# Kernel optimization log

Measured on AMD Instinct MI355X. Metric: run time of the kernel, lower is better.

## Reference

```python
import jax, jax.numpy as jnp
import numpy as np

B, S, IN, OUT, SPLIT = 4, 2048, 4096, 4096, 1024


def setup_inputs() -> dict:
    key = jax.random.key(0)
    ks = jax.random.split(key, 14)
    def n(k, shape, scale=1.0):
        return jax.random.normal(k, shape, dtype=jnp.float32) * scale
    return {
        "x": n(ks[0], (B, S, IN)),
        "V": n(ks[1], (SPLIT, IN)),
        "U": n(ks[2], (OUT, SPLIT)),
        "v2": n(ks[3], (1, IN), 0.05),
        "v1": n(ks[4], (1, SPLIT), 0.05),
        "u2": n(ks[5], (1, SPLIT), 0.05),
        "u1": n(ks[6], (1, OUT), 0.05),
        "V_R": n(ks[7], (SPLIT, IN)),
        "U_R": n(ks[8], (OUT, SPLIT)),
        "v2_R": n(ks[9], (1, IN), 0.05),
        "v1_R": n(ks[10], (1, SPLIT), 0.05),
        "u2_R": n(ks[11], (1, SPLIT), 0.05),
        "u1_R": n(ks[12], (1, OUT), 0.05),
        "bias": n(ks[13], (OUT,), 0.02),
    }


def _quantize(w):
    # ITQ binarization: sign(w) with straight-through estimator semantics
    return w + jax.lax.stop_gradient(jnp.sign(w) - w)


def _compute_forward(x2d, V, U, v2, v1, u2, u1):
    # x2d: [T, in]; V: [split, in]; U: [out, split]
    Vq = _quantize(V)
    Uq = _quantize(U)
    v1u2 = v1 * u2  # [1, split]
    h = (x2d * v2) @ Vq.T          # [T, split]
    return (h * v1u2) @ Uq.T * u1  # [T, out]


def reference(x, V, U, v2, v1, u2, u1, V_R, U_R, v2_R, v1_R, u2_R, u1_R, bias):
    lead = x.shape[:-1]
    x2d = x.reshape(-1, x.shape[-1])
    y = _compute_forward(x2d, V, U, v2, v1, u2, u1)
    y = y + _compute_forward(x2d, V_R, U_R, v2_R, v1_R, u2_R, u1_R)
    y = y + bias
    return y.reshape(lead + (U.shape[0],))
```

## Files before the change

### kernel.cpp

```cpp
#include <hip/hip_runtime.h>


typedef __bf16 bf16x8 __attribute__((ext_vector_type(8)));
typedef float floatx4 __attribute__((ext_vector_type(4)));

__device__ __forceinline__ unsigned short f2bf_rne(float f) {
    union { float f; unsigned u; } v; v.f = f;
    unsigned r = v.u + 0x7FFFu + ((v.u >> 16) & 1u);
    return (unsigned short)(r >> 16);
}

__device__ __forceinline__ float sgnf(float w) {
    return (float)((w > 0.f) - (w < 0.f));
}

__device__ __forceinline__ void async_copy16(const void* g, void* l) {
    __builtin_amdgcn_global_load_lds(
        (const __attribute__((address_space(1))) void*)g,
        (__attribute__((address_space(3))) void*)l, 16, 0, 0);
}

#define FENCE() asm volatile("" ::: "memory")
#define BAR() do { FENCE(); __builtin_amdgcn_s_barrier(); FENCE(); } while (0)
#define VMW(N) asm volatile("s_waitcnt vmcnt(" #N ")" ::: "memory")
#define LGKM(N) asm volatile("s_waitcnt lgkmcnt(" #N ")" ::: "memory")


__global__ void cast_x_kernel(const float* __restrict__ x,
                              unsigned short* __restrict__ xb, int n4) {
    int i = blockIdx.x * blockDim.x + threadIdx.x;
    if (i >= n4) return;
    float4 v = ((const float4*)x)[i];
    ushort4 o;
    o.x = f2bf_rne(v.x); o.y = f2bf_rne(v.y);
    o.z = f2bf_rne(v.z); o.w = f2bf_rne(v.w);
    ((ushort4*)xb)[i] = o;
}

__global__ void prep_w_kernel(const float* __restrict__ V, const float* __restrict__ V_R,
                              const float* __restrict__ v2, const float* __restrict__ v2_R,
                              const float* __restrict__ U, const float* __restrict__ U_R,
                              const float* __restrict__ v1, const float* __restrict__ v1_R,
                              const float* __restrict__ u2, const float* __restrict__ u2_R,
                              const float* __restrict__ u1, const float* __restrict__ u1_R,
                              unsigned short* __restrict__ W1,
                              unsigned short* __restrict__ W2) {
    int bid = blockIdx.x;
    if (bid < 8192) {
        int i = bid * blockDim.x + threadIdx.x;
        int idx = i << 2;
        int scat = idx >> 12;
        int k = idx & 4095;
        const float* Vp; const float* sp;
        if (scat < 1024) { Vp = V + ((size_t)scat << 12); sp = v2; }
        else             { Vp = V_R + ((size_t)(scat - 1024) << 12); sp = v2_R; }
        float4 w = *(const float4*)(Vp + k);
        float4 s = *(const float4*)(sp + k);
        ushort4 o;
        o.x = f2bf_rne(sgnf(w.x) * s.x);
        o.y = f2bf_rne(sgnf(w.y) * s.y);
        o.z = f2bf_rne(sgnf(w.z) * s.z);
        o.w = f2bf_rne(sgnf(w.w) * s.w);
        ((ushort4*)W1)[i] = o;
    } else {
        int i = (bid - 8192) * blockDim.x + threadIdx.x;
        int idx = i << 2;
        int o = idx >> 11;
        int scat = idx & 2047;
        int branch = scat >> 10;
        int s = scat & 1023;
        const float* Up  = branch ? U_R  : U;
        const float* v1p = branch ? v1_R : v1;
        const float* u2p = branch ? u2_R : u2;
        float u1v = (branch ? u1_R : u1)[o];
        float4 w = *(const float4*)(Up + ((size_t)o << 10) + s);
        float4 a = *(const float4*)(v1p + s);
        float4 b = *(const float4*)(u2p + s);
        ushort4 out;
        out.x = f2bf_rne(sgnf(w.x) * a.x * b.x * u1v);
        out.y = f2bf_rne(sgnf(w.y) * a.y * b.y * u1v);
        out.z = f2bf_rne(sgnf(w.z) * a.z * b.z * u1v);
        out.w = f2bf_rne(sgnf(w.w) * a.w * b.w * u1v);
        ((ushort4*)W2)[i] = out;
    }
}


template <bool OUT_BF16, bool ADD_BIAS>
__global__ __launch_bounds__(512, 2)
void gemm256(const unsigned short* __restrict__ A,
             const unsigned short* __restrict__ B,
             void* __restrict__ Cv,
             const float* __restrict__ bias,
             int M, int N, int K, int ntn) {
    (void)M;
    __shared__ __align__(16) unsigned short As[2][2][128 * 64];
    __shared__ __align__(16) unsigned short Bs[2][2][128 * 64];

    const int tid = threadIdx.x;
    const int lane = tid & 63;
    const int wave = tid >> 6;
    const int warp_m = wave >> 2;
    const int warp_n = wave & 3;

    const int nwg = gridDim.x;
    const int hw = blockIdx.x;
    const int swz = (hw & 7) * (nwg >> 3) + (hw >> 3);
    const int tm = swz / ntn;
    const int tn = swz - tm * ntn;
    const int m0 = tm << 8;
    const int n0 = tn << 8;

    const int srow = tid >> 3;
    const int scg8 = (((tid & 7) ^ (srow & 7)) << 3);
    const int ldst = tid << 3;
    const size_t Ks = (size_t)K;

    auto stA = [&](int buf, int h, int kt) {
        const unsigned short* g = A + (size_t)(m0 + (h << 7) + srow) * Ks + (kt << 6) + scg8;
        async_copy16(g,             &As[buf][h][ldst]);
        async_copy16(g + (Ks << 6), &As[buf][h][4096 + ldst]);
    };
    auto stB = [&](int buf, int h, int kt) {
        const unsigned short* g = B + (size_t)(n0 + (h << 7) + srow) * Ks + (kt << 6) + scg8;
        async_copy16(g,             &Bs[buf][h][ldst]);
        async_copy16(g + (Ks << 6), &Bs[buf][h][4096 + ldst]);
    };

    const int fm = lane & 15;
    const int cgl = lane >> 4;
    const int key = fm & 7;
    const int ok0 = ((cgl ^ key) << 3);
    const int ok1 = (((4 | cgl) ^ key) << 3);

    auto lda = [&](bf16x8 (&dst)[4][2], int buf, int mh) {
        const unsigned short* base = &As[buf][warp_m][0];
#pragma unroll
        for (int mi = 0; mi < 4; ++mi) {
            const unsigned short* p = base + (((mh << 6) + (mi << 4) + fm) << 6);
            dst[mi][0] = *(const bf16x8*)(p + ok0);
            dst[mi][1] = *(const bf16x8*)(p + ok1);
        }
    };
    auto ldb = [&](bf16x8 (&dst)[2][2], int buf, int nh) {
        const unsigned short* base = &Bs[buf][warp_n >> 1][0];
#pragma unroll
        for (int ni = 0; ni < 2; ++ni) {
            const unsigned short* p = base + ((((warp_n & 1) << 6) + (nh << 5) + (ni << 4) + fm) << 6);
            dst[ni][0] = *(const bf16x8*)(p + ok0);
            dst[ni][1] = *(const bf16x8*)(p + ok1);
        }
    };

    floatx4 acc[8][4];
#pragma unroll
    for (int i = 0; i < 8; ++i)
#pragma unroll
        for (int j = 0; j < 4; ++j)
#pragma unroll
            for (int r = 0; r < 4; ++r) acc[i][j][r] = 0.f;

    bf16x8 a0[4][2], a1[4][2], b0[2][2], b1[2][2];

#define MMAQ(aS, bS, MH, NH) do { \
    __builtin_amdgcn_s_setprio(1); \
    _Pragma("unroll") \
    for (int mi_ = 0; mi_ < 4; ++mi_) { \
      _Pragma("unroll") \
      for (int ni_ = 0; ni_ < 2; ++ni_) { \
        acc[(MH)*4 + mi_][(NH)*2 + ni_] = __builtin_amdgcn_mfma_f32_16x16x32_bf16( \
            aS[mi_][0], bS[ni_][0], acc[(MH)*4 + mi_][(NH)*2 + ni_], 0, 0, 0); \
        acc[(MH)*4 + mi_][(NH)*2 + ni_] = __builtin_amdgcn_mfma_f32_16x16x32_bf16( \
            aS[mi_][1], bS[ni_][1], acc[(MH)*4 + mi_][(NH)*2 + ni_], 0, 0, 0); \
      } } \
    __builtin_amdgcn_s_setprio(0); \
  } while (0)

    stB(0, 0, 0); stB(0, 1, 0); stA(0, 0, 0); stA(0, 1, 0);
    stB(1, 0, 1); stB(1, 1, 1); stA(1, 0, 1); stA(1, 1, 1);
    VMW(8);
    BAR();

    const int NT = K >> 6;
    for (int i = 0; i < (NT >> 1) - 1; ++i) {
        const int t2k = 2 * i + 2, t3k = 2 * i + 3;
        lda(a0, 0, 0); ldb(b0, 0, 0);
        BAR(); LGKM(0);
        MMAQ(a0, b0, 0, 0);
        BAR();
        ldb(b1, 0, 1);
        BAR(); LGKM(0);
        MMAQ(a0, b1, 0, 1);
        BAR();
        lda(a1, 0, 1);
        stB(0, 0, t2k); stB(0, 1, t2k);
        BAR(); LGKM(0);
        MMAQ(a1, b1, 1, 1);
        BAR();
        stA(0, 0, t2k); stA(0, 1, t2k);
        VMW(8);
        BAR();
        MMAQ(a1, b0, 1, 0);
        BAR();
        lda(a0, 1, 0); ldb(b0, 1, 0);
        BAR(); LGKM(0);
        MMAQ(a0, b0, 0, 0);
        BAR();
        ldb(b1, 1, 1);
        BAR(); LGKM(0);
        MMAQ(a0, b1, 0, 1);
        BAR();
        lda(a1, 1, 1);
        stB(1, 0, t3k); stB(1, 1, t3k);
        BAR(); LGKM(0);
        MMAQ(a1, b1, 1, 1);
        BAR();
        stA(1, 0, t3k); stA(1, 1, t3k);
        VMW(8);
        BAR();
        MMAQ(a1, b0, 1, 0);
        BAR();
    }
    {
        lda(a0, 0, 0); ldb(b0, 0, 0);
        BAR(); LGKM(0);
        MMAQ(a0, b0, 0, 0);
        BAR();
        ldb(b1, 0, 1);
        BAR(); LGKM(0);
        MMAQ(a0, b1, 0, 1);
        BAR();
        lda(a1, 0, 1);
        BAR(); LGKM(0);
        MMAQ(a1, b1, 1, 1);
        BAR();
        VMW(0);
        BAR();
        MMAQ(a1, b0, 1, 0);
        BAR();
        lda(a0, 1, 0); ldb(b0, 1, 0);
        ldb(b1, 1, 1); lda(a1, 1, 1);
        MMAQ(a0, b0, 0, 0);
        MMAQ(a0, b1, 0, 1);
        MMAQ(a1, b1, 1, 1);
        MMAQ(a1, b0, 1, 0);
    }
#undef MMAQ

    const int rq = (lane >> 4) << 2;
    const int col = lane & 15;
#pragma unroll
    for (int mi = 0; mi < 8; ++mi) {
#pragma unroll
        for (int r = 0; r < 4; ++r) {
            const int gm = m0 + (warp_m << 7) + (mi << 4) + rq + r;
            const size_t base = (size_t)gm * (size_t)N;
#pragma unroll
            for (int ni = 0; ni < 4; ++ni) {
                const int gn = n0 + (warp_n << 6) + (ni << 4) + col;
                float v = acc[mi][ni][r];
                if (ADD_BIAS) v += bias[gn];
                if (OUT_BF16)
                    ((unsigned short*)Cv)[base + gn] = f2bf_rne(v);
                else
                    ((float*)Cv)[base + gn] = v;
            }
        }
    }
}


extern "C" void kernel_launch(void* const* d_in, const int* in_sizes, int n_in,
                              void* d_out, int out_size, void* d_ws, size_t ws_size,
                              hipStream_t stream) {
    const float* x    = (const float*)d_in[0];
    const float* V    = (const float*)d_in[1];
    const float* U    = (const float*)d_in[2];
    const float* v2   = (const float*)d_in[3];
    const float* v1   = (const float*)d_in[4];
    const float* u2   = (const float*)d_in[5];
    const float* u1   = (const float*)d_in[6];
    const float* V_R  = (const float*)d_in[7];
    const float* U_R  = (const float*)d_in[8];
    const float* v2_R = (const float*)d_in[9];
    const float* v1_R = (const float*)d_in[10];
    const float* u2_R = (const float*)d_in[11];
    const float* u1_R = (const float*)d_in[12];
    const float* bias = (const float*)d_in[13];
    float* out = (float*)d_out;

    char* ws = (char*)d_ws;
    unsigned short* Xb = (unsigned short*)ws;
    unsigned short* W1 = (unsigned short*)(ws + (size_t)67108864);
    unsigned short* W2 = (unsigned short*)(ws + (size_t)67108864 + 16777216);
    unsigned short* H  = (unsigned short*)(ws + (size_t)67108864 + 33554432);

    cast_x_kernel<<<32768, 256, 0, stream>>>(x, Xb, 8388608);
    prep_w_kernel<<<16384, 256, 0, stream>>>(V, V_R, v2, v2_R,
                                             U, U_R, v1, v1_R, u2, u2_R, u1, u1_R,
                                             W1, W2);

    gemm256<true, false><<<dim3(256), 512, 0, stream>>>(Xb, W1, (void*)H, nullptr,
                                                        8192, 2048, 4096, 8);
    gemm256<false, true><<<dim3(512), 512, 0, stream>>>(H, W2, (void*)out, bias,
                                                        8192, 4096, 2048, 16);
}
```

Before: 536.8 us.

## Merge prep kernels and stagger A-tile global-to-LDS loads across GEMM phases

Combines the x cast and weight prep into a single launch, removing one kernel boundary and its launch gap. In the GEMM main loop, the A-tile async loads for the next stage are now issued one iteration later and spread across sub-phases with adjusted vmcnt/lgkmcnt waits, instead of being issued in bursts alongside the B loads. This aims to overlap memory traffic with MFMA work more evenly. It relies on the LDS buffer reuse timing still being correct, which is a hazard risk if a stA overwrites a half still being read.

```diff
diff --git a/kernel.cpp b/kernel.cpp
--- a/kernel.cpp
+++ b/kernel.cpp
@@ -26,28 +26,26 @@
 #define LGKM(N) asm volatile("s_waitcnt lgkmcnt(" #N ")" ::: "memory")
 
 
-__global__ void cast_x_kernel(const float* __restrict__ x,
-                              unsigned short* __restrict__ xb, int n4) {
-    int i = blockIdx.x * blockDim.x + threadIdx.x;
-    if (i >= n4) return;
-    float4 v = ((const float4*)x)[i];
-    ushort4 o;
-    o.x = f2bf_rne(v.x); o.y = f2bf_rne(v.y);
-    o.z = f2bf_rne(v.z); o.w = f2bf_rne(v.w);
-    ((ushort4*)xb)[i] = o;
-}
-
-__global__ void prep_w_kernel(const float* __restrict__ V, const float* __restrict__ V_R,
-                              const float* __restrict__ v2, const float* __restrict__ v2_R,
-                              const float* __restrict__ U, const float* __restrict__ U_R,
-                              const float* __restrict__ v1, const float* __restrict__ v1_R,
-                              const float* __restrict__ u2, const float* __restrict__ u2_R,
-                              const float* __restrict__ u1, const float* __restrict__ u1_R,
-                              unsigned short* __restrict__ W1,
-                              unsigned short* __restrict__ W2) {
+__global__ void prep_all_kernel(const float* __restrict__ x,
+                                unsigned short* __restrict__ xb,
+                                const float* __restrict__ V, const float* __restrict__ V_R,
+                                const float* __restrict__ v2, const float* __restrict__ v2_R,
+                                const float* __restrict__ U, const float* __restrict__ U_R,
+                                const float* __restrict__ v1, const float* __restrict__ v1_R,
+                                const float* __restrict__ u2, const float* __restrict__ u2_R,
+                                const float* __restrict__ u1, const float* __restrict__ u1_R,
+                                unsigned short* __restrict__ W1,
+                                unsigned short* __restrict__ W2) {
     int bid = blockIdx.x;
-    if (bid < 8192) {
+    if (bid < 32768) {
         int i = bid * blockDim.x + threadIdx.x;
+        float4 v = ((const float4*)x)[i];
+        ushort4 o;
+        o.x = f2bf_rne(v.x); o.y = f2bf_rne(v.y);
+        o.z = f2bf_rne(v.z); o.w = f2bf_rne(v.w);
+        ((ushort4*)xb)[i] = o;
+    } else if (bid < 40960) {
+        int i = (bid - 32768) * blockDim.x + threadIdx.x;
         int idx = i << 2;
         int scat = idx >> 12;
         int k = idx & 4095;
@@ -63,7 +61,7 @@
         o.w = f2bf_rne(sgnf(w.w) * s.w);
         ((ushort4*)W1)[i] = o;
     } else {
-        int i = (bid - 8192) * blockDim.x + threadIdx.x;
+        int i = (bid - 40960) * blockDim.x + threadIdx.x;
         int idx = i << 2;
         int o = idx >> 11;
         int scat = idx & 2047;
@@ -177,56 +175,66 @@
   } while (0)
 
     stB(0, 0, 0); stB(0, 1, 0); stA(0, 0, 0); stA(0, 1, 0);
-    stB(1, 0, 1); stB(1, 1, 1); stA(1, 0, 1); stA(1, 1, 1);
-    VMW(8);
+    stB(1, 0, 1); stB(1, 1, 1);
+    VMW(4);
     BAR();
 
     const int NT = K >> 6;
     for (int i = 0; i < (NT >> 1) - 1; ++i) {
-        const int t2k = 2 * i + 2, t3k = 2 * i + 3;
+        const int t1k = 2 * i + 1, t2k = 2 * i + 2, t3k = 2 * i + 3;
         lda(a0, 0, 0); ldb(b0, 0, 0);
+        stA(1, 0, t1k);
+        LGKM(8);
         BAR(); LGKM(0);
         MMAQ(a0, b0, 0, 0);
         BAR();
         ldb(b1, 0, 1);
+        stA(1, 1, t1k);
         BAR(); LGKM(0);
         MMAQ(a0, b1, 0, 1);
         BAR();
         lda(a1, 0, 1);
-        stB(0, 0, t2k); stB(0, 1, t2k);
+        stB(0, 0, t2k);
         BAR(); LGKM(0);
         MMAQ(a1, b1, 1, 1);
         BAR();
-        stA(0, 0, t2k); stA(0, 1, t2k);
-        VMW(8);
+        stB(0, 1, t2k);
+        VMW(4);
         BAR();
         MMAQ(a1, b0, 1, 0);
         BAR();
         lda(a0, 1, 0); ldb(b0, 1, 0);
+        stA(0, 0, t2k);
+        LGKM(8);
         BAR(); LGKM(0);
         MMAQ(a0, b0, 0, 0);
         BAR();
         ldb(b1, 1, 1);
+        stA(0, 1, t2k);
         BAR(); LGKM(0);
         MMAQ(a0, b1, 0, 1);
         BAR();
         lda(a1, 1, 1);
-        stB(1, 0, t3k); stB(1, 1, t3k);
+        stB(1, 0, t3k);
         BAR(); LGKM(0);
         MMAQ(a1, b1, 1, 1);
         BAR();
-        stA(1, 0, t3k); stA(1, 1, t3k);
-        VMW(8);
+        stB(1, 1, t3k);
+        VMW(4);
         BAR();
         MMAQ(a1, b0, 1, 0);
         BAR();
     }
     {
+        const int tLk = NT - 1;
         lda(a0, 0, 0); ldb(b0, 0, 0);
+        stA(1, 0, tLk);
+        LGKM(8);
         BAR(); LGKM(0);
         MMAQ(a0, b0, 0, 0);
         BAR();
         ldb(b1, 0, 1);
+        stA(1, 1, tLk);
         BAR(); LGKM(0);
         MMAQ(a0, b1, 0, 1);
         BAR();
@@ -295,10 +303,9 @@
     unsigned short* W2 = (unsigned short*)(ws + (size_t)67108864 + 16777216);
     unsigned short* H  = (unsigned short*)(ws + (size_t)67108864 + 33554432);
 
-    cast_x_kernel<<<32768, 256, 0, stream>>>(x, Xb, 8388608);
-    prep_w_kernel<<<16384, 256, 0, stream>>>(V, V_R, v2, v2_R,
-                                             U, U_R, v1, v1_R, u2, u2_R, u1, u1_R,
-                                             W1, W2);
+    prep_all_kernel<<<49152, 256, 0, stream>>>(x, Xb, V, V_R, v2, v2_R,
+                                               U, U_R, v1, v1_R, u2, u2_R, u1, u1_R,
+                                               W1, W2);
 
     gemm256<true, false><<<dim3(256), 512, 0, stream>>>(Xb, W1, (void*)H, nullptr,
                                                         8192, 2048, 4096, 8);
```

Result: no change. 531.9 us (-0.9%).
